# Performance work log

Hardware: AMD Instinct MI355X
Metric: run time of the kernel (lower is better)

Reference implementation:

```python
import jax, jax.numpy as jnp
import numpy as np

HEADS = 16
HIDDEN = 1024
DH = HIDDEN // HEADS
STD = 0.02


def setup_inputs() -> dict:
    key = jax.random.key(0)
    ks = jax.random.split(key, 12)
    B, S = 4, 2048
    inp = {
        'q': jax.random.normal(ks[0], (B, S, HIDDEN), jnp.float32),
        'k': jax.random.normal(ks[1], (B, S, HIDDEN), jnp.float32),
        'v': jax.random.normal(ks[2], (B, S, HIDDEN), jnp.float32),
        'mask': jax.random.randint(ks[3], (B, S), 0, 2, jnp.int32),
        # linear layers: weight [out,in] torch-style, init N(0, 0.02), bias 0
        'wq': STD * jax.random.normal(ks[4], (HIDDEN, HIDDEN), jnp.float32),
        'bq': jnp.zeros((HIDDEN,), jnp.float32),
        'wk': STD * jax.random.normal(ks[5], (HIDDEN, HIDDEN), jnp.float32),
        'bk': jnp.zeros((HIDDEN,), jnp.float32),
        'wv': STD * jax.random.normal(ks[6], (HIDDEN, HIDDEN), jnp.float32),
        'bv': jnp.zeros((HIDDEN,), jnp.float32),
        'wo': STD * jax.random.normal(ks[7], (HIDDEN, HIDDEN), jnp.float32),
        'bo': jnp.zeros((HIDDEN,), jnp.float32),
    }
    return inp


def _split_heads(x):
    B, S, _ = x.shape
    return x.reshape(B, S, HEADS, DH).transpose(0, 2, 1, 3)  # [B,H,S,dh]


def reference(q, k, v, mask, wq, bq, wk, bk, wv, bv, wo, bo):
    B, S, _ = q.shape
    qh = _split_heads(q @ wq.T + bq)
    kh = _split_heads(k @ wk.T + bk)
    vh = _split_heads(v @ wv.T + bv)
    scale = 1.0 / jnp.sqrt(jnp.float32(DH))
    corr = jnp.einsum('bhqd,bhkd->bhqk', qh, kh) * scale  # [B,H,S,S]
    # original masks QUERY rows: mask [B,S] -> [B,1,S,1] broadcast over heads & keys
    row_mask = (mask != 0)[:, None, :, None]
    corr = jnp.where(row_mask, corr, jnp.float32(-1e9))
    prob = jax.nn.softmax(corr, axis=-1)
    # dropout p=0.0 (eval / deterministic reference)
    hidden = jnp.einsum('bhqk,bhkd->bhqd', prob, vh)
    hidden = hidden.transpose(0, 2, 1, 3).reshape(B, S, HIDDEN)
    return hidden @ wo.T + bo
```

## Files before the change

### kernel.cpp

```cpp
#include <hip/hip_runtime.h>

#define BATCH 4
#define SEQ 2048
#define HEADS 16
#define DHEAD 64
#define HID 1024
#define MROWS (BATCH * SEQ)
#define QSCALE 0.1803368801111092f

typedef unsigned short u16;
typedef unsigned int u32;
typedef __attribute__((ext_vector_type(4))) float f32x4;
typedef __attribute__((ext_vector_type(8))) short bf16x8;
typedef __attribute__((ext_vector_type(2))) unsigned int u32x2;
typedef __attribute__((ext_vector_type(4))) unsigned int u32x4;

#define MFMA16(a, b, c) __builtin_amdgcn_mfma_f32_16x16x32_bf16((a), (b), (c), 0, 0, 0)
#define EXP2F(x) __builtin_amdgcn_exp2f(x)

__device__ __forceinline__ u16 f2bf(float f) {
  union { float f; u32 i; } x; x.f = f;
  u32 r = x.i + 0x7fffu + ((x.i >> 16) & 1u);
  return (u16)(r >> 16);
}

__device__ __forceinline__ u32 cvtpk(float a, float b) {
  u32 d;
  asm("v_cvt_pk_bf16_f32 %0, %1, %2" : "=v"(d) : "v"(a), "v"(b));
  return d;
}

__device__ __forceinline__ void lds16(const u16* g, u16* s) {
  __builtin_amdgcn_global_load_lds(
      (const __attribute__((address_space(1))) void*)g,
      (__attribute__((address_space(3))) void*)s, 16, 0, 0);
}

__device__ __forceinline__ void stage8f(const float* __restrict__ g, u16* s) {
  const float4 a = *(const float4*)g;
  const float4 b = *(const float4*)(g + 4);
  ushort4 lo, hi;
  lo.x = f2bf(a.x); lo.y = f2bf(a.y); lo.z = f2bf(a.z); lo.w = f2bf(a.w);
  hi.x = f2bf(b.x); hi.y = f2bf(b.y); hi.z = f2bf(b.z); hi.w = f2bf(b.w);
  *(ushort4*)s = lo;
  *(ushort4*)(s + 4) = hi;
}

struct CvtArgs {
  const float* src[7];
  u16* dst[7];
};
__global__ __launch_bounds__(256) void cvt7(CvtArgs args, int yoff, int nact) {
  const int y = blockIdx.y + yoff;
  const int i = (blockIdx.x * 256 + threadIdx.x) * 8;
  if (y < 3) {
    if (i < nact) stage8f(args.src[y] + i, args.dst[y] + i);
  } else {
    if (i < 4 * (1 << 20)) {
      const int j = i >> 20, off = i & ((1 << 20) - 1);
      stage8f(args.src[3 + j] + off, args.dst[3 + j] + off);
    }
  }
}

template<bool ADMA, bool BDMA>
__device__ __forceinline__ void gemm_core(
    const void* __restrict__ Av, const void* __restrict__ Wv,
    int tid, int m0, int n0, u16* As, u16* Bs, f32x4 (&acc)[4][4])
{
  const int srow = tid >> 2, cslot = tid & 3;
  const int gc = cslot ^ ((srow >> 1) & 3);
  const int w = tid >> 6, l = tid & 63;
  const int quad = l >> 4, l15 = l & 15;
  const int sw = (l15 >> 1) & 3;
  const int wm = (w & 1) << 6, wn = (w >> 1) << 6;

  for (int k0 = 0; k0 < HID; k0 += 32) {
    if (ADMA) {
      const u16* ag = (const u16*)Av + (size_t)(m0 + srow) * HID + k0 + gc * 8;
      lds16(ag, &As[tid * 8]);
      lds16(ag + (size_t)64 * HID, &As[2048 + tid * 8]);
    } else {
      const float* ag = (const float*)Av + (size_t)(m0 + srow) * HID + k0 + gc * 8;
      stage8f(ag, &As[srow * 32 + cslot * 8]);
      stage8f(ag + (size_t)64 * HID, &As[(64 + srow) * 32 + cslot * 8]);
    }
    if (BDMA) {
      const u16* bg = (const u16*)Wv + (size_t)(n0 + srow) * HID + k0 + gc * 8;
      lds16(bg, &Bs[tid * 8]);
      lds16(bg + (size_t)64 * HID, &Bs[2048 + tid * 8]);
    } else {
      const float* bg = (const float*)Wv + (size_t)(n0 + srow) * HID + k0 + gc * 8;
      stage8f(bg, &Bs[srow * 32 + cslot * 8]);
      stage8f(bg + (size_t)64 * HID, &Bs[(64 + srow) * 32 + cslot * 8]);
    }
    __syncthreads();

    bf16x8 a[4], b[4];
    #pragma unroll
    for (int i = 0; i < 4; ++i)
      a[i] = *(const bf16x8*)&As[(wm + i * 16 + l15) * 32 + (quad ^ sw) * 8];
    #pragma unroll
    for (int j = 0; j < 4; ++j)
      b[j] = *(const bf16x8*)&Bs[(wn + j * 16 + l15) * 32 + (quad ^ sw) * 8];
    #pragma unroll
    for (int i = 0; i < 4; ++i)
      #pragma unroll
      for (int j = 0; j < 4; ++j)
        acc[i][j] = MFMA16(a[i], b[j], acc[i][j]);
    __syncthreads();
  }
}

template<bool ADMA, bool BDMA>
__global__ __launch_bounds__(256) void gemm_qkv(
    const void* __restrict__ xq, const void* __restrict__ xk,
    const void* __restrict__ xv,
    const void* __restrict__ wqv, const void* __restrict__ wkv,
    const void* __restrict__ wvv,
    const float* __restrict__ bq, const float* __restrict__ bk,
    const float* __restrict__ bv, const int* __restrict__ Mask,
    u16* __restrict__ qh, u16* __restrict__ kh, u16* __restrict__ vt)
{
  __shared__ u16 As[128 * 32];
  __shared__ u16 Bs[128 * 32];
  const int z = blockIdx.z;
  const void* A = (z == 0) ? xq : (z == 1) ? xk : xv;
  const void* W = (z == 0) ? wqv : (z == 1) ? wkv : wvv;
  const float* Bias = (z == 0) ? bq : (z == 1) ? bk : bv;

  const int tid = threadIdx.x;
  const int m0 = blockIdx.x << 7, n0 = blockIdx.y << 7;
  f32x4 acc[4][4] = {};
  gemm_core<ADMA, BDMA>(A, W, tid, m0, n0, As, Bs, acc);

  const int w = tid >> 6, l = tid & 63;
  const int quad = l >> 4, l15 = l & 15;
  const int wm = (w & 1) << 6, wn = (w >> 1) << 6;

  if (z <= 1) {
    u16* Out = (z == 0) ? qh : kh;
    #pragma unroll
    for (int i = 0; i < 4; ++i) {
      float fl[4];
      #pragma unroll
      for (int r = 0; r < 4; ++r) {
        const int m = m0 + wm + i * 16 + (quad << 2) + r;
        fl[r] = (z == 0) ? (Mask[m] ? QSCALE : 0.f) : 1.f;
      }
      #pragma unroll
      for (int j = 0; j < 4; ++j) {
        const int n = n0 + wn + j * 16 + l15;
        const float bias = Bias[n];
        const int h = n >> 6, d = n & 63;
        #pragma unroll
        for (int r = 0; r < 4; ++r) {
          const int m = m0 + wm + i * 16 + (quad << 2) + r;
          const int bb = m >> 11, s = m & (SEQ - 1);
          Out[((size_t)(bb * HEADS + h) * SEQ + s) * DHEAD + d] =
              f2bf((acc[i][j][r] + bias) * fl[r]);
        }
      }
    }
  } else {
    const int sblk = (m0 + wm) & (SEQ - 1);
    const int bb = (m0 + wm) >> 11;
    #pragma unroll
    for (int j = 0; j < 4; ++j) {
      const int n = n0 + wn + j * 16 + l15;
      const float bias = Bias[n];
      const int h = n >> 6, d = n & 63;
      u16* base = vt + ((size_t)(bb * HEADS + h) * DHEAD + d) * SEQ + sblk;
      #pragma unroll
      for (int r = 0; r < 4; ++r) {
        u32x2 pk;
        pk.x = cvtpk(acc[0][j][r] + bias, acc[1][j][r] + bias);
        pk.y = cvtpk(acc[2][j][r] + bias, acc[3][j][r] + bias);
        *(u32x2*)(base + ((quad << 2) + r) * 4) = pk;
      }
    }
  }
}

template<bool BDMA>
__global__ __launch_bounds__(256) void gemm_out(
    const u16* __restrict__ hidden, const void* __restrict__ wov,
    const float* __restrict__ bo, float* __restrict__ Out)
{
  __shared__ u16 As[128 * 32];
  __shared__ u16 Bs[128 * 32];
  const int tid = threadIdx.x;
  const int m0 = blockIdx.x << 7, n0 = blockIdx.y << 7;
  f32x4 acc[4][4] = {};
  gemm_core<true, BDMA>(hidden, wov, tid, m0, n0, As, Bs, acc);

  const int w = tid >> 6, l = tid & 63;
  const int quad = l >> 4, l15 = l & 15;
  const int wm = (w & 1) << 6, wn = (w >> 1) << 6;
  #pragma unroll
  for (int j = 0; j < 4; ++j) {
    const int n = n0 + wn + j * 16 + l15;
    const float bias = bo[n];
    #pragma unroll
    for (int i = 0; i < 4; ++i) {
      const int mb = m0 + wm + i * 16 + (quad << 2);
      #pragma unroll
      for (int r = 0; r < 4; ++r)
        Out[(size_t)(mb + r) * HID + n] = acc[i][j][r] + bias;
    }
  }
}

__device__ __forceinline__ void core256(
    const u16* __restrict__ A, const u16* __restrict__ W,
    int tid, int m0, int n0, u16* As2, u16* Bs2, f32x4 (&acc)[4][4])
{
  const int l = tid & 63;
  const int quad = l >> 4, l15 = l & 15;
  const int sw7 = l15 & 7;
  const int w = tid >> 6;
  const int wm = (w & 3) << 6, wn = (w >> 2) << 6;
  const int srow = tid >> 3, sslot = tid & 7;
  const int sgc = sslot ^ (srow & 7);

  const u16* aB = A + (size_t)(m0 + srow) * HID + sgc * 8;
  const u16* bB = W + (size_t)(n0 + srow) * HID + sgc * 8;

  #pragma unroll
  for (int tt = 0; tt < 2; ++tt) {
    #pragma unroll
    for (int p = 0; p < 4; ++p)
      lds16(aB + (size_t)p * 64 * HID + tt * 64,
            As2 + tt * 16384 + p * 4096 + tid * 8);
    #pragma unroll
    for (int p = 0; p < 2; ++p)
      lds16(bB + (size_t)p * 64 * HID + tt * 64,
            Bs2 + tt * 8192 + p * 4096 + tid * 8);
  }

  #pragma unroll
  for (int t = 0; t < HID / 64; ++t) {
    if (t < HID / 64 - 1)
      asm volatile("s_waitcnt vmcnt(6)" ::: "memory");
    else
      asm volatile("s_waitcnt vmcnt(0)" ::: "memory");
    __builtin_amdgcn_s_barrier();
    __builtin_amdgcn_sched_barrier(0);

    if (t < HID / 64 - 2) {
      const int kk = (t + 2) << 6;
      u16* ad = As2 + ((t + 2) % 3) * 16384;
      u16* bd = Bs2 + ((t + 2) % 3) * 8192;
      #pragma unroll
      for (int p = 0; p < 4; ++p)
        lds16(aB + (size_t)p * 64 * HID + kk, ad + p * 4096 + tid * 8);
      #pragma unroll
      for (int p = 0; p < 2; ++p)
        lds16(bB + (size_t)p * 64 * HID + kk, bd + p * 4096 + tid * 8);
    }

    const u16* Ab = As2 + (t % 3) * 16384;
    const u16* Bb = Bs2 + (t % 3) * 8192;
    #pragma unroll
    for (int ks = 0; ks < 2; ++ks) {
      const int cc = ((ks << 2) | quad) ^ sw7;
      bf16x8 a[4], b[4];
      #pragma unroll
      for (int i = 0; i < 4; ++i)
        a[i] = *(const bf16x8*)&Ab[(wm + i * 16 + l15) * 64 + cc * 8];
      #pragma unroll
      for (int j = 0; j < 4; ++j)
        b[j] = *(const bf16x8*)&Bb[(wn + j * 16 + l15) * 64 + cc * 8];
      __builtin_amdgcn_s_setprio(1);
      #pragma unroll
      for (int i = 0; i < 4; ++i)
        #pragma unroll
        for (int j = 0; j < 4; ++j)
          acc[i][j] = MFMA16(a[i], b[j], acc[i][j]);
      __builtin_amdgcn_s_setprio(0);
    }
  }
  asm volatile("s_waitcnt vmcnt(0)" ::: "memory");
}

__global__ __launch_bounds__(512, 1) void gemm_qkv2(
    const u16* __restrict__ xq, const u16* __restrict__ xk,
    const u16* __restrict__ xv,
    const u16* __restrict__ wqv, const u16* __restrict__ wkv,
    const u16* __restrict__ wvv,
    const float* __restrict__ bq, const float* __restrict__ bk,
    const float* __restrict__ bv, const int* __restrict__ Mask,
    u16* __restrict__ qh, u16* __restrict__ kh, u16* __restrict__ vt)
{
  __shared__ u16 As2[3 * 16384];
  __shared__ u16 Bs2[3 * 8192];
  const int tid = threadIdx.x;

  const int lin = blockIdx.x;
  const int nid = (lin & 7) * 96 + (lin >> 3);
  const int z = nid >> 8;
  const int rem = nid & 255;
  const int m0 = (rem >> 3) << 8, n0 = (rem & 7) << 7;

  const u16* A = (z == 0) ? xq : (z == 1) ? xk : xv;
  const u16* W = (z == 0) ? wqv : (z == 1) ? wkv : wvv;
  const float* Bias = (z == 0) ? bq : (z == 1) ? bk : bv;

  f32x4 acc[4][4] = {};
  core256(A, W, tid, m0, n0, As2, Bs2, acc);

  const int w = tid >> 6, l = tid & 63;
  const int quad = l >> 4, l15 = l & 15;
  const int wm = (w & 3) << 6, wn = (w >> 2) << 6;

  if (z <= 1) {
    u16* Out = (z == 0) ? qh : kh;
    #pragma unroll
    for (int i = 0; i < 4; ++i) {
      float fl[4];
      #pragma unroll
      for (int r = 0; r < 4; ++r) {
        const int m = m0 + wm + i * 16 + (quad << 2) + r;
        fl[r] = (z == 0) ? (Mask[m] ? QSCALE : 0.f) : 1.f;
      }
      #pragma unroll
      for (int j = 0; j < 4; ++j) {
        const int n = n0 + wn + j * 16 + l15;
        const float bias = Bias[n];
        const int h = n >> 6, d = n & 63;
        #pragma unroll
        for (int r = 0; r < 4; ++r) {
          const int m = m0 + wm + i * 16 + (quad << 2) + r;
          const int bb = m >> 11, s = m & (SEQ - 1);
          Out[((size_t)(bb * HEADS + h) * SEQ + s) * DHEAD + d] =
              f2bf((acc[i][j][r] + bias) * fl[r]);
        }
      }
    }
  } else {
    const int sblk = (m0 + wm) & (SEQ - 1);
    const int bb = (m0 + wm) >> 11;
    #pragma unroll
    for (int j = 0; j < 4; ++j) {
      const int n = n0 + wn + j * 16 + l15;
      const float bias = Bias[n];
      const int h = n >> 6, d = n & 63;
      u16* base = vt + ((size_t)(bb * HEADS + h) * DHEAD + d) * SEQ + sblk;
      #pragma unroll
      for (int r = 0; r < 4; ++r) {
        u32x2 pk;
        pk.x = cvtpk(acc[0][j][r] + bias, acc[1][j][r] + bias);
        pk.y = cvtpk(acc[2][j][r] + bias, acc[3][j][r] + bias);
        *(u32x2*)(base + ((quad << 2) + r) * 4) = pk;
      }
    }
  }
}

__global__ __launch_bounds__(512, 1) void gemm_out2(
    const u16* __restrict__ hidden, const u16* __restrict__ wov,
    const float* __restrict__ bo, float* __restrict__ Out)
{
  __shared__ u16 As2[3 * 16384];
  __shared__ u16 Bs2[3 * 8192];
  const int tid = threadIdx.x;

  const int lin = blockIdx.x;
  const int nid = (lin & 7) * 32 + (lin >> 3);
  const int m0 = (nid >> 3) << 8, n0 = (nid & 7) << 7;

  f32x4 acc[4][4] = {};
  core256(hidden, wov, tid, m0, n0, As2, Bs2, acc);

  const int w = tid >> 6, l = tid & 63;
  const int quad = l >> 4, l15 = l & 15;
  const int wm = (w & 3) << 6, wn = (w >> 2) << 6;
  #pragma unroll
  for (int j = 0; j < 4; ++j) {
    const int n = n0 + wn + j * 16 + l15;
    const float bias = bo[n];
    #pragma unroll
    for (int i = 0; i < 4; ++i) {
      const int mb = m0 + wm + i * 16 + (quad << 2);
      #pragma unroll
      for (int r = 0; r < 4; ++r)
        Out[(size_t)(mb + r) * HID + n] = acc[i][j][r] + bias;
    }
  }
}

__global__ __launch_bounds__(128, 2) void attn_mfma(
    const u16* __restrict__ QH, const u16* __restrict__ KH,
    const u16* __restrict__ VT, u16* __restrict__ Hidden)
{
  __shared__ u16 Ks[2][2048];
  __shared__ u16 Vt[2][4096];

  const int tid = threadIdx.x;
  const int w = tid >> 6, l = tid & 63;
  const int quad = l >> 4, l15 = l & 15;
  const int sw = (l15 >> 1) & 3;
  const int srow = tid >> 2, cslot = tid & 3;
  const int gc = cslot ^ ((srow >> 1) & 3);
  const int vd = tid >> 3;
  const int vc = (tid & 7) ^ (vd & 7);

  const int lin = blockIdx.y * 16 + blockIdx.x;
  const int bh = lin & 63, b = bh >> 4, h = bh & 15;
  const int q0 = (lin >> 6) << 7;

  const u16* qbase = QH + (size_t)bh * SEQ * DHEAD;
  const u16* kbase = KH + (size_t)bh * SEQ * DHEAD;
  const u16* vbase = VT + (size_t)bh * DHEAD * SEQ;

  bf16x8 aq[2][4];
  #pragma unroll
  for (int hh = 0; hh < 2; ++hh)
    #pragma unroll
    for (int j = 0; j < 4; ++j)
      aq[hh][j] = *(const bf16x8*)(qbase +
          (size_t)(q0 + w * 64 + j * 16 + l15) * DHEAD + hh * 32 + quad * 8);
  asm volatile("s_waitcnt vmcnt(0)" ::: "memory");

  #pragma unroll
  for (int hh = 0; hh < 2; ++hh)
    #pragma unroll
    for (int part = 0; part < 2; ++part)
      lds16(kbase + (size_t)(part * 32 + srow) * DHEAD + hh * 32 + gc * 8,
            &Ks[hh][part * 1024 + tid * 8]);
  #pragma unroll
  for (int part = 0; part < 4; ++part)
    lds16(vbase + (size_t)(part * 16 + vd) * SEQ + vc * 8,
          &Vt[0][part * 1024 + tid * 8]);

  const bf16x8 ones8 = {0x3F80, 0x3F80, 0x3F80, 0x3F80,
                        0x3F80, 0x3F80, 0x3F80, 0x3F80};
  f32x4 o[4][4] = {};
  f32x4 lacc[4] = {};
  int cur = 0;

  for (int it = 0; it < SEQ / 64; ++it) {
    asm volatile("s_waitcnt vmcnt(4)" ::: "memory");
    __builtin_amdgcn_s_barrier();

    f32x4 s[4][4] = {};
    __builtin_amdgcn_s_setprio(1);
    #pragma unroll
    for (int i = 0; i < 4; ++i)
      #pragma unroll
      for (int hh = 0; hh < 2; ++hh) {
        const bf16x8 ak = *(const bf16x8*)
            &Ks[hh][(i * 16 + l15) * 32 + (quad ^ sw) * 8];
        #pragma unroll
        for (int j = 0; j < 4; ++j)
          s[i][j] = MFMA16(ak, aq[hh][j], s[i][j]);
      }
    __builtin_amdgcn_s_setprio(0);
    __builtin_amdgcn_s_barrier();

    const int tn = ((it + 1) & (SEQ / 64 - 1)) << 6;
    #pragma unroll
    for (int hh = 0; hh < 2; ++hh)
      #pragma unroll
      for (int part = 0; part < 2; ++part)
        lds16(kbase + (size_t)(tn + part * 32 + srow) * DHEAD + hh * 32 + gc * 8,
              &Ks[hh][part * 1024 + tid * 8]);
    #pragma unroll
    for (int part = 0; part < 4; ++part)
      lds16(vbase + (size_t)(part * 16 + vd) * SEQ + tn + vc * 8,
            &Vt[cur ^ 1][part * 1024 + tid * 8]);

    bf16x8 bp[2][4];
    #pragma unroll
    for (int j = 0; j < 4; ++j) {
      float p[4][4];
      #pragma unroll
      for (int i = 0; i < 4; ++i)
        #pragma unroll
        for (int r = 0; r < 4; ++r)
          p[i][r] = EXP2F(s[i][j][r]);
      u32x4 t0, t1;
      t0.x = cvtpk(p[0][0], p[1][0]); t0.y = cvtpk(p[2][0], p[3][0]);
      t0.z = cvtpk(p[0][1], p[1][1]); t0.w = cvtpk(p[2][1], p[3][1]);
      t1.x = cvtpk(p[0][2], p[1][2]); t1.y = cvtpk(p[2][2], p[3][2]);
      t1.z = cvtpk(p[0][3], p[1][3]); t1.w = cvtpk(p[2][3], p[3][3]);
      bp[0][j] = __builtin_bit_cast(bf16x8, t0);
      bp[1][j] = __builtin_bit_cast(bf16x8, t1);
      lacc[j] = MFMA16(ones8, bp[0][j], lacc[j]);
      lacc[j] = MFMA16(ones8, bp[1][j], lacc[j]);
    }

    asm volatile("s_waitcnt vmcnt(8)" ::: "memory");
    __builtin_amdgcn_s_barrier();

    __builtin_amdgcn_s_setprio(1);
    #pragma unroll
    for (int hh = 0; hh < 2; ++hh)
      #pragma unroll
      for (int m = 0; m < 4; ++m) {
        const int d = m * 16 + l15;
        const bf16x8 av = *(const bf16x8*)
            &Vt[cur][d * 64 + (((quad * 2 + hh) ^ (d & 7)) << 3)];
        #pragma unroll
        for (int j = 0; j < 4; ++j)
          o[m][j] = MFMA16(av, bp[hh][j], o[m][j]);
      }
    __builtin_amdgcn_s_setprio(0);
    cur ^= 1;
  }
  asm volatile("s_waitcnt vmcnt(0)" ::: "memory");

  float inv[4];
  #pragma unroll
  for (int j = 0; j < 4; ++j)
    inv[j] = 1.f / lacc[j][0];

  #pragma unroll
  for (int m = 0; m < 4; ++m)
    #pragma unroll
    for (int j = 0; j < 4; ++j) {
      u32x2 pk;
      pk.x = cvtpk(o[m][j][0] * inv[j], o[m][j][1] * inv[j]);
      pk.y = cvtpk(o[m][j][2] * inv[j], o[m][j][3] * inv[j]);
      *(u32x2*)&Hidden[(size_t)(b * SEQ + q0 + w * 64 + j * 16 + l15) * HID
                       + h * DHEAD + m * 16 + quad * 4] = pk;
    }
}

extern "C" void kernel_launch(void* const* d_in, const int* in_sizes, int n_in,
                              void* d_out, int out_size, void* d_ws, size_t ws_size,
                              hipStream_t stream) {
  const float* q  = (const float*)d_in[0];
  const float* k  = (const float*)d_in[1];
  const float* v  = (const float*)d_in[2];
  const int* mask = (const int*)d_in[3];
  const float* wq = (const float*)d_in[4];
  const float* bq = (const float*)d_in[5];
  const float* wk = (const float*)d_in[6];
  const float* bk = (const float*)d_in[7];
  const float* wv = (const float*)d_in[8];
  const float* bv = (const float*)d_in[9];
  const float* wo = (const float*)d_in[10];
  const float* bo = (const float*)d_in[11];

  const size_t SEG = (size_t)MROWS * HID;
  const size_t WSEG = (size_t)HID * HID;
  const dim3 gq(MROWS / 128, HID / 128, 3);
  const dim3 go(MROWS / 128, HID / 128);
  const dim3 ga(SEQ / 128, BATCH * HEADS);

  const size_t planFULL = (6 * SEG + 4 * WSEG) * sizeof(u16);
  const size_t planMID  = (4 * SEG + 4 * WSEG) * sizeof(u16);

  if (ws_size >= planFULL) {
    u16* qb  = (u16*)d_ws;
    u16* kb  = qb + SEG;
    u16* vb  = kb + SEG;
    u16* qh  = vb + SEG;
    u16* kh  = qh + SEG;
    u16* vt  = kh + SEG;
    u16* wqb = vt + SEG;
    u16* wkb = wqb + WSEG;
    u16* wvb = wkb + WSEG;
    u16* wob = wvb + WSEG;
    u16* hidden = qb;

    CvtArgs ca;
    ca.src[0] = q;  ca.dst[0] = qb;
    ca.src[1] = k;  ca.dst[1] = kb;
    ca.src[2] = v;  ca.dst[2] = vb;
    ca.src[3] = wq; ca.dst[3] = wqb;
    ca.src[4] = wk; ca.dst[4] = wkb;
    ca.src[5] = wv; ca.dst[5] = wvb;
    ca.src[6] = wo; ca.dst[6] = wob;
    cvt7<<<dim3(SEG / 2048, 4), 256, 0, stream>>>(ca, 0, (int)SEG);

    gemm_qkv2<<<dim3(768), 512, 0, stream>>>(qb, kb, vb, wqb, wkb, wvb,
                                             bq, bk, bv, mask, qh, kh, vt);
    attn_mfma<<<ga, 128, 0, stream>>>(qh, kh, vt, hidden);
    gemm_out2<<<dim3(256), 512, 0, stream>>>(hidden, wob, bo, (float*)d_out);
  } else if (ws_size >= planMID) {
    u16* wqb = (u16*)d_ws;
    u16* wkb = wqb + WSEG;
    u16* wvb = wkb + WSEG;
    u16* wob = wvb + WSEG;
    u16* qh = wob + WSEG;
    u16* kh = qh + SEG;
    u16* vt = kh + SEG;
    u16* hidden = vt + SEG;

    CvtArgs ca;
    ca.src[0] = ca.src[1] = ca.src[2] = q;
    ca.dst[0] = ca.dst[1] = ca.dst[2] = wqb;
    ca.src[3] = wq; ca.dst[3] = wqb;
    ca.src[4] = wk; ca.dst[4] = wkb;
    ca.src[5] = wv; ca.dst[5] = wvb;
    ca.src[6] = wo; ca.dst[6] = wob;
    cvt7<<<dim3(4 * WSEG / 2048, 1), 256, 0, stream>>>(ca, 3, 0);

    gemm_qkv<false, true><<<gq, 256, 0, stream>>>(q, k, v, wqb, wkb, wvb,
                                                  bq, bk, bv, mask, qh, kh, vt);
    attn_mfma<<<ga, 128, 0, stream>>>(qh, kh, vt, hidden);
    gemm_out<true><<<go, 256, 0, stream>>>(hidden, wob, bo, (float*)d_out);
  } else {
    u16* qh = (u16*)d_ws;
    u16* kh = qh + SEG;
    u16* vt = kh + SEG;
    u16* hidden = vt + SEG;

    gemm_qkv<false, false><<<gq, 256, 0, stream>>>(q, k, v, wq, wk, wv,
                                                   bq, bk, bv, mask, qh, kh, vt);
    attn_mfma<<<ga, 128, 0, stream>>>(qh, kh, vt, hidden);
    gemm_out<false><<<go, 256, 0, stream>>>(hidden, wo, bo, (float*)d_out);
  }
}
```

Measured before the change: 325.3 us.

## Replace QKV projection GEMM with 256x256 tile, ping-pong LDS pipelined kernel

```diff
diff --git a/kernel.cpp b/kernel.cpp
--- a/kernel.cpp
+++ b/kernel.cpp
@@ -283,7 +283,7 @@
   asm volatile("s_waitcnt vmcnt(0)" ::: "memory");
 }
 
-__global__ __launch_bounds__(512, 1) void gemm_qkv2(
+__global__ __launch_bounds__(512, 1) void gemm_qkv3(
     const u16* __restrict__ xq, const u16* __restrict__ xk,
     const u16* __restrict__ xv,
     const u16* __restrict__ wqv, const u16* __restrict__ wkv,
@@ -292,45 +292,149 @@
     const float* __restrict__ bv, const int* __restrict__ Mask,
     u16* __restrict__ qh, u16* __restrict__ kh, u16* __restrict__ vt)
 {
-  __shared__ u16 As2[3 * 16384];
-  __shared__ u16 Bs2[3 * 8192];
+  __shared__ u16 As3[2][2][8192];
+  __shared__ u16 Bs3[2][2][8192];
+
   const int tid = threadIdx.x;
+  const int l = tid & 63;
+  const int quad = l >> 4, l15 = l & 15;
+  const int sw7 = l15 & 7;
+  const int wid = tid >> 6;
+  const int wavem = wid & 1, waven = wid >> 1;
+  const int srow8 = tid >> 3;
+  const int schunk = (tid & 7) ^ (srow8 & 7);
 
   const int lin = blockIdx.x;
-  const int nid = (lin & 7) * 96 + (lin >> 3);
-  const int z = nid >> 8;
-  const int rem = nid & 255;
-  const int m0 = (rem >> 3) << 8, n0 = (rem & 7) << 7;
+  const int nid = (lin & 7) * 48 + (lin >> 3);
+  const int z = nid >> 7;
+  const int rem = nid & 127;
+  const int m0 = (rem >> 2) << 8, n0 = (rem & 3) << 8;
 
   const u16* A = (z == 0) ? xq : (z == 1) ? xk : xv;
   const u16* W = (z == 0) ? wqv : (z == 1) ? wkv : wvv;
   const float* Bias = (z == 0) ? bq : (z == 1) ? bk : bv;
 
-  f32x4 acc[4][4] = {};
-  core256(A, W, tid, m0, n0, As2, Bs2, acc);
-
-  const int w = tid >> 6, l = tid & 63;
-  const int quad = l >> 4, l15 = l & 15;
-  const int wm = (w & 3) << 6, wn = (w >> 2) << 6;
+  const u16* aG = A + (size_t)(m0 + srow8) * HID + schunk * 8;
+  const u16* bG = W + (size_t)(n0 + srow8) * HID + schunk * 8;
+
+#define ST_A(tt, hh) do { \
+    lds16(aG + (size_t)((hh) * 128) * HID + (tt) * 64, \
+          &As3[(tt) & 1][hh][tid * 8]); \
+    lds16(aG + (size_t)((hh) * 128 + 64) * HID + (tt) * 64, \
+          &As3[(tt) & 1][hh][4096 + tid * 8]); \
+  } while (0)
+#define ST_B(tt, hh) do { \
+    lds16(bG + (size_t)((hh) * 128) * HID + (tt) * 64, \
+          &Bs3[(tt) & 1][hh][tid * 8]); \
+    lds16(bG + (size_t)((hh) * 128 + 64) * HID + (tt) * 64, \
+          &Bs3[(tt) & 1][hh][4096 + tid * 8]); \
+  } while (0)
+#define BARSB() do { __builtin_amdgcn_s_barrier(); \
+                     __builtin_amdgcn_sched_barrier(0); } while (0)
+
+  f32x4 acc[8][4] = {};
+
+  ST_B(0, 0); ST_B(0, 1); ST_A(0, 0); ST_A(0, 1); ST_B(1, 0);
+  asm volatile("s_waitcnt vmcnt(2)" ::: "memory");
+  BARSB();
+
+  const int bro = (waven & 1) * 64;
+
+  #pragma unroll
+  for (int t = 0; t < HID / 64; ++t) {
+    const int p = t & 1;
+    const u16* Ah = &As3[p][wavem][0];
+    const u16* Bh = &Bs3[p][waven >> 1][0];
+    bf16x8 a[4], b[4];
+
+    #pragma unroll
+    for (int j = 0; j < 4; ++j)
+      b[j] = *(const bf16x8*)&Bh[(bro + j * 16 + l15) * 64 + (quad ^ sw7) * 8];
+    #pragma unroll
+    for (int m = 0; m < 4; ++m)
+      a[m] = *(const bf16x8*)&Ah[(m * 16 + l15) * 64 + (quad ^ sw7) * 8];
+    if (t + 1 < HID / 64) ST_B(t + 1, 1);
+    BARSB();
+    __builtin_amdgcn_s_setprio(1);
+    #pragma unroll
+    for (int m = 0; m < 4; ++m)
+      #pragma unroll
+      for (int j = 0; j < 4; ++j)
+        acc[m][j] = MFMA16(a[m], b[j], acc[m][j]);
+    __builtin_amdgcn_s_setprio(0);
+    BARSB();
+
+    #pragma unroll
+    for (int m = 0; m < 4; ++m)
+      a[m] = *(const bf16x8*)&Ah[(64 + m * 16 + l15) * 64 + (quad ^ sw7) * 8];
+    if (t + 1 < HID / 64) ST_A(t + 1, 0);
+    BARSB();
+    __builtin_amdgcn_s_setprio(1);
+    #pragma unroll
+    for (int m = 0; m < 4; ++m)
+      #pragma unroll
+      for (int j = 0; j < 4; ++j)
+        acc[4 + m][j] = MFMA16(a[m], b[j], acc[4 + m][j]);
+    __builtin_amdgcn_s_setprio(0);
+    BARSB();
+
+    #pragma unroll
+    for (int j = 0; j < 4; ++j)
+      b[j] = *(const bf16x8*)&Bh[(bro + j * 16 + l15) * 64 + ((4 | quad) ^ sw7) * 8];
+    #pragma unroll
+    for (int m = 0; m < 4; ++m)
+      a[m] = *(const bf16x8*)&Ah[(m * 16 + l15) * 64 + ((4 | quad) ^ sw7) * 8];
+    if (t + 1 < HID / 64) ST_A(t + 1, 1);
+    BARSB();
+    __builtin_amdgcn_s_setprio(1);
+    #pragma unroll
+    for (int m = 0; m < 4; ++m)
+      #pragma unroll
+      for (int j = 0; j < 4; ++j)
+        acc[m][j] = MFMA16(a[m], b[j], acc[m][j]);
+    __builtin_amdgcn_s_setprio(0);
+    BARSB();
+
+    #pragma unroll
+    for (int m = 0; m < 4; ++m)
+      a[m] = *(const bf16x8*)&Ah[(64 + m * 16 + l15) * 64 + ((4 | quad) ^ sw7) * 8];
+    if (t + 2 < HID / 64) ST_B(t + 2, 0);
+    BARSB();
+    __builtin_amdgcn_s_setprio(1);
+    #pragma unroll
+    for (int m = 0; m < 4; ++m)
+      #pragma unroll
+      for (int j = 0; j < 4; ++j)
+        acc[4 + m][j] = MFMA16(a[m], b[j], acc[4 + m][j]);
+    __builtin_amdgcn_s_setprio(0);
+    if (t + 2 < HID / 64)
+      asm volatile("s_waitcnt vmcnt(2)" ::: "memory");
+    else
+      asm volatile("s_waitcnt vmcnt(0)" ::: "memory");
+    BARSB();
+  }
+#undef ST_A
+#undef ST_B
+#undef BARSB
 
   if (z <= 1) {
     u16* Out = (z == 0) ? qh : kh;
     #pragma unroll
-    for (int i = 0; i < 4; ++i) {
+    for (int i = 0; i < 8; ++i) {
       float fl[4];
       #pragma unroll
       for (int r = 0; r < 4; ++r) {
-        const int m = m0 + wm + i * 16 + (quad << 2) + r;
+        const int m = m0 + wavem * 128 + i * 16 + (quad << 2) + r;
         fl[r] = (z == 0) ? (Mask[m] ? QSCALE : 0.f) : 1.f;
       }
       #pragma unroll
       for (int j = 0; j < 4; ++j) {
-        const int n = n0 + wn + j * 16 + l15;
+        const int n = n0 + waven * 64 + j * 16 + l15;
         const float bias = Bias[n];
         const int h = n >> 6, d = n & 63;
         #pragma unroll
         for (int r = 0; r < 4; ++r) {
-          const int m = m0 + wm + i * 16 + (quad << 2) + r;
+          const int m = m0 + wavem * 128 + i * 16 + (quad << 2) + r;
           const int bb = m >> 11, s = m & (SEQ - 1);
           Out[((size_t)(bb * HEADS + h) * SEQ + s) * DHEAD + d] =
               f2bf((acc[i][j][r] + bias) * fl[r]);
@@ -338,20 +442,26 @@
       }
     }
   } else {
-    const int sblk = (m0 + wm) & (SEQ - 1);
-    const int bb = (m0 + wm) >> 11;
-    #pragma unroll
-    for (int j = 0; j < 4; ++j) {
-      const int n = n0 + wn + j * 16 + l15;
-      const float bias = Bias[n];
-      const int h = n >> 6, d = n & 63;
-      u16* base = vt + ((size_t)(bb * HEADS + h) * DHEAD + d) * SEQ + sblk;
-      #pragma unroll
-      for (int r = 0; r < 4; ++r) {
-        u32x2 pk;
-        pk.x = cvtpk(acc[0][j][r] + bias, acc[1][j][r] + bias);
-        pk.y = cvtpk(acc[2][j][r] + bias, acc[3][j][r] + bias);
-        *(u32x2*)(base + ((quad << 2) + r) * 4) = pk;
+    #pragma unroll
+    for (int ig = 0; ig < 2; ++ig) {
+      const int mbase = m0 + wavem * 128 + ig * 64;
+      const int sblk = mbase & (SEQ - 1);
+      const int bb = mbase >> 11;
+      #pragma unroll
+      for (int j = 0; j < 4; ++j) {
+        const int n = n0 + waven * 64 + j * 16 + l15;
+        const float bias = Bias[n];
+        const int h = n >> 6, d = n & 63;
+        u16* base = vt + ((size_t)(bb * HEADS + h) * DHEAD + d) * SEQ + sblk;
+        #pragma unroll
+        for (int r = 0; r < 4; ++r) {
+          u32x2 pk;
+          pk.x = cvtpk(acc[ig * 4 + 0][j][r] + bias,
+                       acc[ig * 4 + 1][j][r] + bias);
+          pk.y = cvtpk(acc[ig * 4 + 2][j][r] + bias,
+                       acc[ig * 4 + 3][j][r] + bias);
+          *(u32x2*)(base + ((quad << 2) + r) * 4) = pk;
+        }
       }
     }
   }
@@ -575,7 +685,7 @@
     ca.src[6] = wo; ca.dst[6] = wob;
     cvt7<<<dim3(SEG / 2048, 4), 256, 0, stream>>>(ca, 0, (int)SEG);
 
-    gemm_qkv2<<<dim3(768), 512, 0, stream>>>(qb, kb, vb, wqb, wkb, wvb,
+    gemm_qkv3<<<dim3(384), 512, 0, stream>>>(qb, kb, vb, wqb, wkb, wvb,
                                              bq, bk, bv, mask, qh, kh, vt);
     attn_mfma<<<ga, 128, 0, stream>>>(qh, kh, vt, hidden);
     gemm_out2<<<dim3(256), 512, 0, stream>>>(hidden, wob, bo, (float*)d_out);
```

New measurement: 333.2 us. 2.4% more time.
